# Kernel tuning notes

Hardware: AMD Instinct MI355X
Metric: run time of the kernel (lower is better)

The kernel has to match this reference:

```python
import jax, jax.numpy as jnp
import numpy as np

N = 8192
IN_F = 512
OUT_F = 128
ALPHA = 0.2  # leaky relu negative slope
NEG_BIG = -1e10
RND_SCALE = 1e5


def setup_inputs() -> dict:
    key = jax.random.key(0)
    k1, k2, k3, k4, k5 = jax.random.split(key, 5)
    h = jax.random.normal(k1, (N, IN_F), dtype=jnp.float32)
    adj = jax.random.randint(k2, (N, N), 0, 2, dtype=jnp.int32)
    W = jax.random.normal(k3, (IN_F, OUT_F), dtype=jnp.float32) * 0.05
    a = jax.random.normal(k4, (2 * OUT_F, 1), dtype=jnp.float32) * 0.1
    # rnd in original is 1e5*(rand-0.5); same distribution here
    rnd = RND_SCALE * (jax.random.uniform(k5, (N, OUT_F), dtype=jnp.float32) - 0.5)
    return {"h": h, "adj": adj, "W": W, "a": a, "rnd": rnd}


def reference(h, adj, W, a, rnd):
    Wh = h @ W                              # [N, OUT_F]
    Wh1 = Wh @ a[:OUT_F, :]                 # [N, 1]
    Wh2 = Wh @ a[OUT_F:, :]                 # [N, 1]
    e = jax.nn.leaky_relu(Wh1 + Wh2.T, negative_slope=ALPHA)  # [N, N]
    attention = jnp.where(adj > 0, e, NEG_BIG)
    attention = jax.nn.softmax(attention, axis=1)
    h_prime = attention @ Wh                # [N, OUT_F]
    h_prime = (h_prime + rnd) / RND_SCALE
    return jax.nn.elu(h_prime)
```

## Files before the change

### kernel.cpp

```cpp
#include <hip/hip_runtime.h>

#define N 8192
#define IN_F 512
#define OUT_F 128
#define SPLITK 16
#define LOG2E 1.4426950408889634f
#define LN2 0.6931471805599453f

typedef __attribute__((ext_vector_type(4))) float f32x4;
typedef __attribute__((ext_vector_type(8))) short bf16x8;
typedef __attribute__((ext_vector_type(8))) unsigned short u16x8;

__device__ __forceinline__ short f2bf(float f) {
    union { float f; unsigned u; } c; c.f = f;
    unsigned r = c.u + 0x7FFFu + ((c.u >> 16) & 1u);
    return (short)(r >> 16);
}

__device__ __forceinline__ float exp2fast(float x) {
#if __has_builtin(__builtin_amdgcn_exp2f)
    return __builtin_amdgcn_exp2f(x);
#else
    return __expf(x * LN2);
#endif
}

__global__ __launch_bounds__(256) void conv_W(const float* __restrict__ W, short* __restrict__ WT) {
    int idx = blockIdx.x * 256 + threadIdx.x;
    int n = idx & (OUT_F - 1);
    int k = idx >> 7;
    WT[(size_t)n * IN_F + k] = f2bf(W[idx]);
}

__global__ __launch_bounds__(256) void gemm_hW(const float* __restrict__ h,
                                               const short* __restrict__ WT,
                                               const float* __restrict__ a,
                                               short* __restrict__ WhT,
                                               float* __restrict__ sOut,
                                               float* __restrict__ tOut) {
    const int tid = threadIdx.x;
    const int wave = tid >> 6, lane = tid & 63;
    const int row16 = lane & 15, kgrp = lane >> 4;
    const int m0 = blockIdx.x * 16;
    const int kbase = wave * 128;

    f32x4 acc[8] = {};
    const float4* hp = (const float4*)(h + (size_t)(m0 + row16) * IN_F + kbase);

#pragma unroll
    for (int kk = 0; kk < 128; kk += 32) {
        float4 u0 = hp[kk / 4 + kgrp * 2];
        float4 u1 = hp[kk / 4 + kgrp * 2 + 1];
        bf16x8 af;
        af[0] = f2bf(u0.x); af[1] = f2bf(u0.y); af[2] = f2bf(u0.z); af[3] = f2bf(u0.w);
        af[4] = f2bf(u1.x); af[5] = f2bf(u1.y); af[6] = f2bf(u1.z); af[7] = f2bf(u1.w);
#pragma unroll
        for (int nt = 0; nt < 8; nt++) {
            bf16x8 bf_ = *(const bf16x8*)(WT + (size_t)(nt * 16 + row16) * IN_F + kbase + kk + kgrp * 8);
            acc[nt] = __builtin_amdgcn_mfma_f32_16x16x32_bf16(af, bf_, acc[nt], 0, 0, 0);
        }
    }

    __shared__ float red[4][16][132];
#pragma unroll
    for (int nt = 0; nt < 8; nt++)
#pragma unroll
        for (int r = 0; r < 4; r++)
            red[wave][kgrp * 4 + r][nt * 16 + row16] = acc[nt][r];
    __syncthreads();

    const int row = tid >> 4, seg = tid & 15;
    float v[8];
#pragma unroll
    for (int e = 0; e < 8; e++) {
        int c = seg * 8 + e;
        v[e] = red[0][row][c] + red[1][row][c] + red[2][row][c] + red[3][row][c];
    }
    float sp = 0.f, tp = 0.f;
#pragma unroll
    for (int e = 0; e < 8; e++) {
        sp += v[e] * a[seg * 8 + e];
        tp += v[e] * a[OUT_F + seg * 8 + e];
    }
    sp += __shfl_xor(sp, 1); tp += __shfl_xor(tp, 1);
    sp += __shfl_xor(sp, 2); tp += __shfl_xor(tp, 2);
    sp += __shfl_xor(sp, 4); tp += __shfl_xor(tp, 4);
    sp += __shfl_xor(sp, 8); tp += __shfl_xor(tp, 8);
    if (seg == 0) {
        sOut[m0 + row] = sp * LOG2E;
        tOut[m0 + row] = tp * LOG2E;
    }
#pragma unroll
    for (int e = 0; e < 8; e++)
        WhT[(size_t)(seg * 8 + e) * N + m0 + row] = f2bf(v[e]);
}

__global__ __launch_bounds__(512, 2) void attn(const int* __restrict__ adj,
                                               const short* __restrict__ WhT,
                                               const float* __restrict__ s,
                                               const float* __restrict__ t,
                                               unsigned short* __restrict__ num,
                                               float* __restrict__ lpart) {
    const int tid = threadIdx.x;
    const int wave = tid >> 6, lane = tid & 63;
    const int row16 = lane & 15, kgrp = lane >> 4;
    const int m0 = blockIdx.x * 256 + wave * 32;
    const int ks = blockIdx.y * 512;

    __shared__ float tl[512];
    if (tid < 512) tl[tid] = t[ks + tid];
    __syncthreads();

    float s_m[2];
    const int4* ap[2];
#pragma unroll
    for (int mi = 0; mi < 2; mi++) {
        int m = m0 + mi * 16 + row16;
        s_m[mi] = s[m];
        ap[mi] = (const int4*)(adj + (size_t)m * N + ks) + kgrp * 2;
    }

    f32x4 acc[2][8] = {};
    float lsum[2] = {0.f, 0.f};

    int4 buf[2][2][2];
#pragma unroll
    for (int mi = 0; mi < 2; mi++)
#pragma unroll
        for (int q = 0; q < 2; q++) {
            buf[0][mi][q] = ap[mi][q];
            buf[1][mi][q] = ap[mi][8 + q];
        }

#pragma unroll 2
    for (int c = 0; c < 16; c++) {
        int4 cur[2][2];
#pragma unroll
        for (int mi = 0; mi < 2; mi++)
#pragma unroll
            for (int q = 0; q < 2; q++) cur[mi][q] = buf[c & 1][mi][q];
        if (c < 14) {
#pragma unroll
            for (int mi = 0; mi < 2; mi++)
#pragma unroll
                for (int q = 0; q < 2; q++) buf[c & 1][mi][q] = ap[mi][(c + 2) * 8 + q];
        }

        const float* tp = tl + c * 32 + kgrp * 8;
        float4 tA = *(const float4*)tp;
        float4 tB = *(const float4*)(tp + 4);
        float tv[8] = { tA.x, tA.y, tA.z, tA.w, tB.x, tB.y, tB.z, tB.w };

        bf16x8 bfr[8];
        const short* bb = WhT + ks + c * 32 + kgrp * 8;
#pragma unroll
        for (int ni = 0; ni < 8; ni++)
            bfr[ni] = *(const bf16x8*)(bb + (size_t)(ni * 16 + row16) * N);

#pragma unroll
        for (int mi = 0; mi < 2; mi++) {
            const int* ai = (const int*)cur[mi];
            unsigned pu[8];
#pragma unroll
            for (int e = 0; e < 8; e++) {
                float x = s_m[mi] + tv[e];
                x = fmaxf(x, 0.2f * x);
                float p = exp2fast(x);
                unsigned u = __float_as_uint(p) & 0xFFFF0000u;
                u = ai[e] > 0 ? u : 0u;
                lsum[mi] += __uint_as_float(u);
                pu[e] = u;
            }
            bf16x8 af;
            unsigned* au = (unsigned*)&af;
#pragma unroll
            for (int q = 0; q < 4; q++) au[q] = (pu[2 * q] >> 16) | pu[2 * q + 1];
#pragma unroll
            for (int ni = 0; ni < 8; ni++)
                acc[mi][ni] = __builtin_amdgcn_mfma_f32_16x16x32_bf16(af, bfr[ni], acc[mi][ni], 0, 0, 0);
        }
    }

#pragma unroll
    for (int mi = 0; mi < 2; mi++) {
        float v = lsum[mi];
        v += __shfl_xor(v, 16);
        v += __shfl_xor(v, 32);
        if (kgrp == 0) lpart[(size_t)blockIdx.y * N + m0 + mi * 16 + row16] = v;
    }

    unsigned short* np_ = num + (size_t)blockIdx.y * N * OUT_F;
#pragma unroll
    for (int mi = 0; mi < 2; mi++) {
        int mb = m0 + mi * 16 + kgrp * 4;
#pragma unroll
        for (int ni = 0; ni < 8; ni++) {
            int n = ni * 16 + row16;
#pragma unroll
            for (int r = 0; r < 4; r++)
                np_[(size_t)(mb + r) * OUT_F + n] = (unsigned short)f2bf(acc[mi][ni][r]);
        }
    }
}

__global__ __launch_bounds__(256) void finalize(const unsigned short* __restrict__ num,
                                                const float* __restrict__ lpart,
                                                const float* __restrict__ rnd,
                                                float* __restrict__ out) {
    int idx = blockIdx.x * 256 + threadIdx.x;
    int m = idx >> 4;
    int c = (idx & 15) * 8;
    size_t g = (size_t)m * OUT_F + c;

    float nm[8] = {};
#pragma unroll
    for (int bk = 0; bk < SPLITK; bk++) {
        u16x8 v = *(const u16x8*)(num + (size_t)bk * N * OUT_F + g);
#pragma unroll
        for (int e = 0; e < 8; e++) nm[e] += __uint_as_float((unsigned)v[e] << 16);
    }
    float l = 0.f;
#pragma unroll
    for (int bk = 0; bk < SPLITK; bk++) l += lpart[(size_t)bk * N + m];
    float inv = 1.f / fmaxf(l, 1e-30f);

    float4 r0 = *(const float4*)(rnd + g);
    float4 r1 = *(const float4*)(rnd + g + 4);
    float rv[8] = { r0.x, r0.y, r0.z, r0.w, r1.x, r1.y, r1.z, r1.w };
    float ov[8];
#pragma unroll
    for (int e = 0; e < 8; e++) {
        float x = (nm[e] * inv + rv[e]) * 1e-5f;
        ov[e] = x > 0.f ? x : __expf(x) - 1.f;
    }
    *(float4*)(out + g)     = make_float4(ov[0], ov[1], ov[2], ov[3]);
    *(float4*)(out + g + 4) = make_float4(ov[4], ov[5], ov[6], ov[7]);
}

extern "C" void kernel_launch(void* const* d_in, const int* in_sizes, int n_in,
                              void* d_out, int out_size, void* d_ws, size_t ws_size,
                              hipStream_t stream) {
    const float* h   = (const float*)d_in[0];
    const int*   adj = (const int*)d_in[1];
    const float* W   = (const float*)d_in[2];
    const float* a   = (const float*)d_in[3];
    const float* rnd = (const float*)d_in[4];
    float* out = (float*)d_out;

    char* w = (char*)d_ws;
    short* WT    = (short*)(w);
    short* WhT   = (short*)(w + 131072);
    float* sv    = (float*)(w + 2228224);
    float* tv    = (float*)(w + 2260992);
    float* lpart = (float*)(w + 2293760);
    unsigned short* num = (unsigned short*)(w + 2818048);

    conv_W  <<<256, 256, 0, stream>>>(W, WT);
    gemm_hW <<<512, 256, 0, stream>>>(h, WT, a, WhT, sv, tv);
    attn    <<<dim3(32, SPLITK), 512, 0, stream>>>(adj, WhT, sv, tv, num, lpart);
    finalize<<<(N * OUT_F / 8) / 256, 256, 0, stream>>>(num, lpart, rnd, out);
}
```

Baseline: 457.0 us.

## Stage WhT tiles into LDS via async global-to-LDS loads with double buffering

```diff
diff --git a/kernel.cpp b/kernel.cpp
--- a/kernel.cpp
+++ b/kernel.cpp
@@ -23,6 +23,12 @@
 #else
     return __expf(x * LN2);
 #endif
+}
+
+__device__ __forceinline__ void load_lds16(const void* g, void* l) {
+    __builtin_amdgcn_global_load_lds((const __attribute__((address_space(1))) unsigned*)g,
+                                     (__attribute__((address_space(3))) unsigned*)l,
+                                     16, 0, 0);
 }
 
 __global__ __launch_bounds__(256) void conv_W(const float* __restrict__ W, short* __restrict__ WT) {
@@ -95,7 +101,7 @@
         WhT[(size_t)(seg * 8 + e) * N + m0 + row] = f2bf(v[e]);
 }
 
-__global__ __launch_bounds__(512, 2) void attn(const int* __restrict__ adj,
+__global__ __launch_bounds__(256, 3) void attn(const int* __restrict__ adj,
                                                const short* __restrict__ WhT,
                                                const float* __restrict__ s,
                                                const float* __restrict__ t,
@@ -104,81 +110,101 @@
     const int tid = threadIdx.x;
     const int wave = tid >> 6, lane = tid & 63;
     const int row16 = lane & 15, kgrp = lane >> 4;
-    const int m0 = blockIdx.x * 256 + wave * 32;
+    const int m0 = blockIdx.x * 128 + wave * 32;
     const int ks = blockIdx.y * 512;
 
+    __shared__ short Bs[2][2][128 * 32];
     __shared__ float tl[512];
-    if (tid < 512) tl[tid] = t[ks + tid];
-    __syncthreads();
+
+    tl[tid] = t[ks + tid];
+    if (tid < 256) tl[tid + 256] = t[ks + tid + 256];
 
     float s_m[2];
-    const int4* ap[2];
+    const int4* ap4[2];
 #pragma unroll
     for (int mi = 0; mi < 2; mi++) {
         int m = m0 + mi * 16 + row16;
         s_m[mi] = s[m];
-        ap[mi] = (const int4*)(adj + (size_t)m * N + ks) + kgrp * 2;
-    }
+        ap4[mi] = (const int4*)(adj + (size_t)m * N + ks);
+    }
+
+    auto stageB = [&](int sup, int par) {
+        const int k0 = ks + sup * 64;
+#pragma unroll
+        for (int d = 0; d < 2; d++)
+#pragma unroll
+            for (int q = 0; q < 2; q++) {
+                int nrow = wave * 32 + q * 16 + (lane >> 2);
+                const short* g = WhT + (size_t)nrow * N + k0 + d * 32 + (lane & 3) * 8;
+                load_lds16(g, &Bs[par][d][(wave * 32 + q * 16) * 32]);
+            }
+    };
 
     f32x4 acc[2][8] = {};
     float lsum[2] = {0.f, 0.f};
 
-    int4 buf[2][2][2];
+    int4 nx[2][2];
 #pragma unroll
     for (int mi = 0; mi < 2; mi++)
 #pragma unroll
-        for (int q = 0; q < 2; q++) {
-            buf[0][mi][q] = ap[mi][q];
-            buf[1][mi][q] = ap[mi][8 + q];
+        for (int q = 0; q < 2; q++) nx[mi][q] = ap4[mi][kgrp * 2 + q];
+    stageB(0, 0);
+    __syncthreads();
+
+    for (int sp = 0; sp < 8; sp++) {
+        const int par = sp & 1;
+#pragma unroll
+        for (int d = 0; d < 2; d++) {
+            const int g = sp * 2 + d;
+            int4 cu[2][2];
+#pragma unroll
+            for (int mi = 0; mi < 2; mi++)
+#pragma unroll
+                for (int q = 0; q < 2; q++) cu[mi][q] = nx[mi][q];
+            if (g + 1 < 16) {
+#pragma unroll
+                for (int mi = 0; mi < 2; mi++)
+#pragma unroll
+                    for (int q = 0; q < 2; q++)
+                        nx[mi][q] = ap4[mi][(g + 1) * 8 + kgrp * 2 + q];
+            }
+            if (d == 0 && sp + 1 < 8) stageB(sp + 1, par ^ 1);
+
+            const float* tp = tl + g * 32 + kgrp * 8;
+            float4 tA = *(const float4*)tp;
+            float4 tB = *(const float4*)(tp + 4);
+            float tv[8] = { tA.x, tA.y, tA.z, tA.w, tB.x, tB.y, tB.z, tB.w };
+
+            bf16x8 bfr[8];
+            const short* base = &Bs[par][d][0];
+#pragma unroll
+            for (int ni = 0; ni < 8; ni++)
+                bfr[ni] = *(const bf16x8*)(base + (ni * 16 + row16) * 32 + kgrp * 8);
+
+#pragma unroll
+            for (int mi = 0; mi < 2; mi++) {
+                const int* ai = (const int*)cu[mi];
+                unsigned pu[8];
+#pragma unroll
+                for (int e = 0; e < 8; e++) {
+                    float x = s_m[mi] + tv[e];
+                    x = fmaxf(x, 0.2f * x);
+                    float p = exp2fast(x);
+                    unsigned u = __float_as_uint(p) & 0xFFFF0000u;
+                    u = ai[e] > 0 ? u : 0u;
+                    lsum[mi] += __uint_as_float(u);
+                    pu[e] = u;
+                }
+                bf16x8 af;
+                unsigned* au = (unsigned*)&af;
+#pragma unroll
+                for (int q = 0; q < 4; q++) au[q] = (pu[2 * q] >> 16) | pu[2 * q + 1];
+#pragma unroll
+                for (int ni = 0; ni < 8; ni++)
+                    acc[mi][ni] = __builtin_amdgcn_mfma_f32_16x16x32_bf16(af, bfr[ni], acc[mi][ni], 0, 0, 0);
+            }
         }
-
-#pragma unroll 2
-    for (int c = 0; c < 16; c++) {
-        int4 cur[2][2];
-#pragma unroll
-        for (int mi = 0; mi < 2; mi++)
-#pragma unroll
-            for (int q = 0; q < 2; q++) cur[mi][q] = buf[c & 1][mi][q];
-        if (c < 14) {
-#pragma unroll
-            for (int mi = 0; mi < 2; mi++)
-#pragma unroll
-                for (int q = 0; q < 2; q++) buf[c & 1][mi][q] = ap[mi][(c + 2) * 8 + q];
-        }
-
-        const float* tp = tl + c * 32 + kgrp * 8;
-        float4 tA = *(const float4*)tp;
-        float4 tB = *(const float4*)(tp + 4);
-        float tv[8] = { tA.x, tA.y, tA.z, tA.w, tB.x, tB.y, tB.z, tB.w };
-
-        bf16x8 bfr[8];
-        const short* bb = WhT + ks + c * 32 + kgrp * 8;
-#pragma unroll
-        for (int ni = 0; ni < 8; ni++)
-            bfr[ni] = *(const bf16x8*)(bb + (size_t)(ni * 16 + row16) * N);
-
-#pragma unroll
-        for (int mi = 0; mi < 2; mi++) {
-            const int* ai = (const int*)cur[mi];
-            unsigned pu[8];
-#pragma unroll
-            for (int e = 0; e < 8; e++) {
-                float x = s_m[mi] + tv[e];
-                x = fmaxf(x, 0.2f * x);
-                float p = exp2fast(x);
-                unsigned u = __float_as_uint(p) & 0xFFFF0000u;
-                u = ai[e] > 0 ? u : 0u;
-                lsum[mi] += __uint_as_float(u);
-                pu[e] = u;
-            }
-            bf16x8 af;
-            unsigned* au = (unsigned*)&af;
-#pragma unroll
-            for (int q = 0; q < 4; q++) au[q] = (pu[2 * q] >> 16) | pu[2 * q + 1];
-#pragma unroll
-            for (int ni = 0; ni < 8; ni++)
-                acc[mi][ni] = __builtin_amdgcn_mfma_f32_16x16x32_bf16(af, bfr[ni], acc[mi][ni], 0, 0, 0);
-        }
+        __syncthreads();
     }
 
 #pragma unroll
@@ -257,6 +283,6 @@
 
     conv_W  <<<256, 256, 0, stream>>>(W, WT);
     gemm_hW <<<512, 256, 0, stream>>>(h, WT, a, WhT, sv, tv);
-    attn    <<<dim3(32, SPLITK), 512, 0, stream>>>(adj, WhT, sv, tv, num, lpart);
+    attn    <<<dim3(64, SPLITK), 256, 0, stream>>>(adj, WhT, sv, tv, num, lpart);
     finalize<<<(N * OUT_F / 8) / 256, 256, 0, stream>>>(num, lpart, rnd, out);
 }
```

Result: faster. 441.4 us (-3.4%).

## Pack adjacency into bitmask and restructure attention split-K with register-pipelined B

Applied to the files above, without the earlier changes.

```diff
diff --git a/kernel.cpp b/kernel.cpp
--- a/kernel.cpp
+++ b/kernel.cpp
@@ -3,7 +3,9 @@
 #define N 8192
 #define IN_F 512
 #define OUT_F 128
-#define SPLITK 16
+#define NW (N / 8)
+#define SPLITK 8
+#define KC 1024
 #define LOG2E 1.4426950408889634f
 #define LN2 0.6931471805599453f
 
@@ -30,6 +32,24 @@
     int n = idx & (OUT_F - 1);
     int k = idx >> 7;
     WT[(size_t)n * IN_F + k] = f2bf(W[idx]);
+}
+
+__global__ __launch_bounds__(256) void mkmask(const int* __restrict__ adj,
+                                              unsigned char* __restrict__ maskR) {
+    const int wave = threadIdx.x >> 6, lane = threadIdx.x & 63;
+    const size_t m = (size_t)blockIdx.x * 4 + wave;
+    const int4* ap = (const int4*)(adj + m * N);
+    unsigned char* mp = maskR + m * NW;
+#pragma unroll 4
+    for (int it = 0; it < 16; it++) {
+        int b4 = it * 128 + lane * 2;
+        int4 a0 = ap[b4], a1 = ap[b4 + 1];
+        unsigned b = (unsigned)(a0.x > 0) | ((unsigned)(a0.y > 0) << 1) |
+                     ((unsigned)(a0.z > 0) << 2) | ((unsigned)(a0.w > 0) << 3) |
+                     ((unsigned)(a1.x > 0) << 4) | ((unsigned)(a1.y > 0) << 5) |
+                     ((unsigned)(a1.z > 0) << 6) | ((unsigned)(a1.w > 0) << 7);
+        mp[it * 64 + lane] = (unsigned char)b;
+    }
 }
 
 __global__ __launch_bounds__(256) void gemm_hW(const float* __restrict__ h,
@@ -95,7 +115,7 @@
         WhT[(size_t)(seg * 8 + e) * N + m0 + row] = f2bf(v[e]);
 }
 
-__global__ __launch_bounds__(512, 2) void attn(const int* __restrict__ adj,
+__global__ __launch_bounds__(256, 2) void attn(const unsigned char* __restrict__ maskR,
                                                const short* __restrict__ WhT,
                                                const float* __restrict__ s,
                                                const float* __restrict__ t,
@@ -104,80 +124,77 @@
     const int tid = threadIdx.x;
     const int wave = tid >> 6, lane = tid & 63;
     const int row16 = lane & 15, kgrp = lane >> 4;
-    const int m0 = blockIdx.x * 256 + wave * 32;
-    const int ks = blockIdx.y * 512;
-
-    __shared__ float tl[512];
-    if (tid < 512) tl[tid] = t[ks + tid];
-    __syncthreads();
+    const int mw = blockIdx.x * 128 + wave * 32;
+    const int ks = blockIdx.y * KC;
 
     float s_m[2];
-    const int4* ap[2];
+    const int4* mp[2];
 #pragma unroll
     for (int mi = 0; mi < 2; mi++) {
-        int m = m0 + mi * 16 + row16;
+        int m = mw + mi * 16 + row16;
         s_m[mi] = s[m];
-        ap[mi] = (const int4*)(adj + (size_t)m * N + ks) + kgrp * 2;
-    }
+        mp[mi] = (const int4*)(maskR + (size_t)m * NW + (ks >> 3));
+    }
+
+    const short* Bbase = WhT + ks + kgrp * 8;
+    bf16x8 Bb[2][8];
+#pragma unroll
+    for (int ni = 0; ni < 8; ni++) {
+        Bb[0][ni] = *(const bf16x8*)(Bbase + (size_t)(ni * 16 + row16) * N);
+        Bb[1][ni] = *(const bf16x8*)(Bbase + (size_t)(ni * 16 + row16) * N + 32);
+    }
+
+    int4 mcur[2], mnxt[2];
+#pragma unroll
+    for (int mi = 0; mi < 2; mi++) { mcur[mi] = mp[mi][0]; mnxt[mi] = mp[mi][1]; }
 
     f32x4 acc[2][8] = {};
     float lsum[2] = {0.f, 0.f};
-
-    int4 buf[2][2][2];
-#pragma unroll
-    for (int mi = 0; mi < 2; mi++)
-#pragma unroll
-        for (int q = 0; q < 2; q++) {
-            buf[0][mi][q] = ap[mi][q];
-            buf[1][mi][q] = ap[mi][8 + q];
-        }
-
-#pragma unroll 2
-    for (int c = 0; c < 16; c++) {
-        int4 cur[2][2];
-#pragma unroll
-        for (int mi = 0; mi < 2; mi++)
-#pragma unroll
-            for (int q = 0; q < 2; q++) cur[mi][q] = buf[c & 1][mi][q];
-        if (c < 14) {
-#pragma unroll
-            for (int mi = 0; mi < 2; mi++)
-#pragma unroll
-                for (int q = 0; q < 2; q++) buf[c & 1][mi][q] = ap[mi][(c + 2) * 8 + q];
-        }
-
-        const float* tp = tl + c * 32 + kgrp * 8;
-        float4 tA = *(const float4*)tp;
-        float4 tB = *(const float4*)(tp + 4);
-        float tv[8] = { tA.x, tA.y, tA.z, tA.w, tB.x, tB.y, tB.z, tB.w };
-
-        bf16x8 bfr[8];
-        const short* bb = WhT + ks + c * 32 + kgrp * 8;
-#pragma unroll
-        for (int ni = 0; ni < 8; ni++)
-            bfr[ni] = *(const bf16x8*)(bb + (size_t)(ni * 16 + row16) * N);
-
-#pragma unroll
-        for (int mi = 0; mi < 2; mi++) {
-            const int* ai = (const int*)cur[mi];
-            unsigned pu[8];
-#pragma unroll
-            for (int e = 0; e < 8; e++) {
-                float x = s_m[mi] + tv[e];
-                x = fmaxf(x, 0.2f * x);
-                float p = exp2fast(x);
-                unsigned u = __float_as_uint(p) & 0xFFFF0000u;
-                u = ai[e] > 0 ? u : 0u;
-                lsum[mi] += __uint_as_float(u);
-                pu[e] = u;
+    const float* tbase = t + ks + kgrp * 8;
+
+#pragma unroll
+    for (int a = 0; a < 8; a++) {
+        int4 mk[2];
+#pragma unroll
+        for (int mi = 0; mi < 2; mi++) { mk[mi] = mcur[mi]; mcur[mi] = mnxt[mi]; }
+        if (a + 2 < 8) {
+#pragma unroll
+            for (int mi = 0; mi < 2; mi++) mnxt[mi] = mp[mi][a + 2];
+        }
+#pragma unroll
+        for (int d = 0; d < 4; d++) {
+            const int g = a * 4 + d;
+            float4 tA = *(const float4*)(tbase + g * 32);
+            float4 tB = *(const float4*)(tbase + g * 32 + 4);
+            float tv[8] = { tA.x, tA.y, tA.z, tA.w, tB.x, tB.y, tB.z, tB.w };
+
+#pragma unroll
+            for (int mi = 0; mi < 2; mi++) {
+                const unsigned mbyte = ((unsigned)((const int*)&mk[mi])[d] >> (kgrp * 8)) & 0xFFu;
+                unsigned pu[8];
+#pragma unroll
+                for (int e = 0; e < 8; e++) {
+                    float x = s_m[mi] + tv[e];
+                    x = fmaxf(x, 0.2f * x);
+                    float p = exp2fast(x);
+                    unsigned u = __float_as_uint(p) & 0xFFFF0000u;
+                    u = ((mbyte >> e) & 1u) ? u : 0u;
+                    lsum[mi] += __uint_as_float(u);
+                    pu[e] = u;
+                }
+                bf16x8 af;
+                unsigned* au = (unsigned*)&af;
+#pragma unroll
+                for (int q = 0; q < 4; q++) au[q] = (pu[2 * q] >> 16) | pu[2 * q + 1];
+#pragma unroll
+                for (int ni = 0; ni < 8; ni++)
+                    acc[mi][ni] = __builtin_amdgcn_mfma_f32_16x16x32_bf16(af, Bb[g & 1][ni], acc[mi][ni], 0, 0, 0);
             }
-            bf16x8 af;
-            unsigned* au = (unsigned*)&af;
-#pragma unroll
-            for (int q = 0; q < 4; q++) au[q] = (pu[2 * q] >> 16) | pu[2 * q + 1];
-#pragma unroll
-            for (int ni = 0; ni < 8; ni++)
-                acc[mi][ni] = __builtin_amdgcn_mfma_f32_16x16x32_bf16(af, bfr[ni], acc[mi][ni], 0, 0, 0);
+            if (g + 2 < 32) {
+#pragma unroll
+                for (int ni = 0; ni < 8; ni++)
+                    Bb[g & 1][ni] = *(const bf16x8*)(Bbase + (size_t)(ni * 16 + row16) * N + (g + 2) * 32);
+            }
         }
     }
 
@@ -186,19 +203,18 @@
         float v = lsum[mi];
         v += __shfl_xor(v, 16);
         v += __shfl_xor(v, 32);
-        if (kgrp == 0) lpart[(size_t)blockIdx.y * N + m0 + mi * 16 + row16] = v;
-    }
-
-    unsigned short* np_ = num + (size_t)blockIdx.y * N * OUT_F;
+        if (kgrp == 0) lpart[(size_t)blockIdx.y * N + mw + mi * 16 + row16] = v;
+    }
+
+    unsigned short* np_ = num + ((size_t)blockIdx.y * N + mw) * OUT_F;
 #pragma unroll
     for (int mi = 0; mi < 2; mi++) {
-        int mb = m0 + mi * 16 + kgrp * 4;
 #pragma unroll
         for (int ni = 0; ni < 8; ni++) {
             int n = ni * 16 + row16;
 #pragma unroll
             for (int r = 0; r < 4; r++)
-                np_[(size_t)(mb + r) * OUT_F + n] = (unsigned short)f2bf(acc[mi][ni][r]);
+                np_[(size_t)(mi * 16 + kgrp * 4 + r) * OUT_F + n] = (unsigned short)f2bf(acc[mi][ni][r]);
         }
     }
 }
@@ -253,10 +269,12 @@
     float* sv    = (float*)(w + 2228224);
     float* tv    = (float*)(w + 2260992);
     float* lpart = (float*)(w + 2293760);
-    unsigned short* num = (unsigned short*)(w + 2818048);
+    unsigned char* maskR = (unsigned char*)(w + 2555904);
+    unsigned short* num  = (unsigned short*)(w + 10944512);
 
     conv_W  <<<256, 256, 0, stream>>>(W, WT);
+    mkmask  <<<2048, 256, 0, stream>>>(adj, maskR);
     gemm_hW <<<512, 256, 0, stream>>>(h, WT, a, WhT, sv, tv);
-    attn    <<<dim3(32, SPLITK), 512, 0, stream>>>(adj, WhT, sv, tv, num, lpart);
+    attn    <<<dim3(64, SPLITK), 256, 0, stream>>>(maskR, WhT, sv, tv, num, lpart);
     finalize<<<(N * OUT_F / 8) / 256, 256, 0, stream>>>(num, lpart, rnd, out);
 }
```

Result: slower. 509.8 us (+11.6%).
